# Optimization experiments

Hardware: AMD Instinct MI355X
Metric: run time of the kernel (lower is better)

## Reference

```python
import jax, jax.numpy as jnp
import numpy as np

D_MODEL = 1024
HID = 4096  # d_model * att_size
N_KEYS = 65536
TOP_K = 6


def setup_inputs() -> dict:
    root = jax.random.key(0)
    k0, k1, k2, k3, k4, k5 = jax.random.split(root, 6)
    s = 1.0 / np.sqrt(D_MODEL)
    return {
        "query": jax.random.normal(k0, (D_MODEL,), dtype=jnp.float32),
        "key_mat": jax.random.normal(k1, (N_KEYS, D_MODEL), dtype=jnp.float32),
        "Wq": jax.random.normal(k2, (HID, D_MODEL), dtype=jnp.float32) * s,
        "bq": jax.random.normal(k3, (HID,), dtype=jnp.float32) * s,
        "Wk": jax.random.normal(k4, (HID, D_MODEL), dtype=jnp.float32) * s,
        "bk": jax.random.normal(k5, (HID,), dtype=jnp.float32) * s,
    }


def reference(query, key_mat, Wq, bq, Wk, bk):
    # Linear projections (nn.Linear: x @ W^T + b)
    q = jnp.dot(Wq, query) + bq                 # [HID]
    k = jnp.dot(key_mat, Wk.T) + bk             # [N, HID]
    scores = jnp.dot(k, q)                      # [N]
    # The torch loop does k=6 sequential argmax + mask(-100000) + gather,
    # which (absent pathological -100000 scores) is exactly top-6 selection.
    _, idx = jax.lax.top_k(scores, TOP_K)       # [TOP_K]
    return jnp.mean(key_mat[idx], axis=0)       # [D_MODEL]
```

## Files before the change

### kernel.cpp

```cpp
#include <hip/hip_runtime.h>

#define DM    1024
#define HID   4096
#define NKEYS 65536
#define TOPK  6
#define NEGF  (-3.4e38f)

typedef float fvec4 __attribute__((ext_vector_type(4)));

__device__ __forceinline__ fvec4 nt_load4(const float* p) {
    return __builtin_nontemporal_load((const fvec4*)p);
}

__global__ __launch_bounds__(256) void qproj_kernel(const float* __restrict__ Wq,
                                                    const float* __restrict__ query,
                                                    const float* __restrict__ bq,
                                                    float* __restrict__ q) {
    const int wave = threadIdx.x >> 6;
    const int lane = threadIdx.x & 63;
    const int h = blockIdx.x * 4 + wave;
    const float* Wrow = Wq + (size_t)h * DM;
    const fvec4* __restrict__ qv = (const fvec4*)query;
    float acc = 0.f;
#pragma unroll
    for (int k = 0; k < 4; ++k) {
        fvec4 w = nt_load4(Wrow + (lane + k * 64) * 4);
        fvec4 x = qv[lane + k * 64];
        acc += w.x * x.x + w.y * x.y + w.z * x.z + w.w * x.w;
    }
#pragma unroll
    for (int off = 32; off > 0; off >>= 1) acc += __shfl_down(acc, off);
    if (lane == 0) q[h] = acc + bq[h];
}

__global__ __launch_bounds__(256) void vproj_kernel(const float* __restrict__ Wk,
                                                    const float* __restrict__ q,
                                                    float* __restrict__ v_part) {
    const int t  = threadIdx.x;
    const int b  = blockIdx.x;
    const int h0 = b * 16;
    fvec4 acc = {0.f, 0.f, 0.f, 0.f};
#pragma unroll 4
    for (int j = 0; j < 16; ++j) {
        const int h = h0 + j;
        const float qh = q[h];
        fvec4 w = nt_load4(Wk + (size_t)h * DM + t * 4);
        acc += w * qh;
    }
    *(fvec4*)(v_part + (size_t)b * DM + t * 4) = acc;
}

__global__ __launch_bounds__(64) void vreduce_kernel(const float* __restrict__ v_part,
                                                     float* __restrict__ v) {
    const int d = blockIdx.x * 64 + threadIdx.x;
    float acc = 0.f;
#pragma unroll 8
    for (int b = 0; b < 256; ++b) acc += v_part[(size_t)b * DM + d];
    v[d] = acc;
}

__global__ __launch_bounds__(256) void score_kernel(const float* __restrict__ key_mat,
                                                    const float* __restrict__ v,
                                                    float* __restrict__ scores) {
    const int wave = threadIdx.x >> 6;
    const int lane = threadIdx.x & 63;
    const int r = blockIdx.x * 4 + wave;
    const float* row = key_mat + (size_t)r * DM;
    const fvec4* __restrict__ vv = (const fvec4*)v;
    float acc = 0.f;
#pragma unroll
    for (int k = 0; k < 4; ++k) {
        fvec4 a = nt_load4(row + (lane + k * 64) * 4);
        fvec4 b = vv[lane + k * 64];
        acc += a.x * b.x + a.y * b.y + a.z * b.z + a.w * b.w;
    }
#pragma unroll
    for (int off = 32; off > 0; off >>= 1) acc += __shfl_down(acc, off);
    if (lane == 0) scores[r] = acc;
}

__global__ __launch_bounds__(256) void topk_stage1(const float* __restrict__ scores,
                                                   float* __restrict__ cand_v,
                                                   int* __restrict__ cand_i) {
    const int t = threadIdx.x, b = blockIdx.x;
    const int i = b * 256 + t;
    float cur = scores[i];

    __shared__ float wv[4];
    __shared__ int   wi[4];
    __shared__ float selv[TOPK];
    __shared__ int   seli[TOPK];

    for (int p = 0; p < TOPK; ++p) {
        float m = cur; int mi = i;
#pragma unroll
        for (int off = 32; off > 0; off >>= 1) {
            float ov = __shfl_down(m, off);
            int   oi = __shfl_down(mi, off);
            if (ov > m) { m = ov; mi = oi; }
        }
        const int lane = t & 63, w = t >> 6;
        if (lane == 0) { wv[w] = m; wi[w] = mi; }
        __syncthreads();
        if (t == 0) {
            float bm = wv[0]; int bix = wi[0];
#pragma unroll
            for (int j = 1; j < 4; ++j) if (wv[j] > bm) { bm = wv[j]; bix = wi[j]; }
            selv[p] = bm; seli[p] = bix;
        }
        __syncthreads();
        if (i == seli[p]) cur = NEGF;
    }
    if (t < TOPK) { cand_v[b * TOPK + t] = selv[t]; cand_i[b * TOPK + t] = seli[t]; }
}

__global__ __launch_bounds__(256) void topk_stage2_mean(const float* __restrict__ cand_v,
                                                        const int* __restrict__ cand_i,
                                                        const float* __restrict__ key_mat,
                                                        float* __restrict__ out) {
    const int t = threadIdx.x;
    const int NC = 256 * TOPK;

    __shared__ float sv[NC];
    __shared__ int   si[NC];
    __shared__ float wv[4];
    __shared__ int   wi[4];
    __shared__ int   sel[TOPK];

#pragma unroll
    for (int j = 0; j < TOPK; ++j) {
        sv[t + j * 256] = cand_v[t + j * 256];
        si[t + j * 256] = cand_i[t + j * 256];
    }
    __syncthreads();

    for (int p = 0; p < TOPK; ++p) {
        float m = NEGF; int mp = 0;
#pragma unroll
        for (int j = 0; j < TOPK; ++j) {
            const int pos = t * TOPK + j;
            const float val = sv[pos];
            if (val > m) { m = val; mp = pos; }
        }
#pragma unroll
        for (int off = 32; off > 0; off >>= 1) {
            float ov = __shfl_down(m, off);
            int   op = __shfl_down(mp, off);
            if (ov > m) { m = ov; mp = op; }
        }
        const int lane = t & 63, w = t >> 6;
        if (lane == 0) { wv[w] = m; wi[w] = mp; }
        __syncthreads();
        if (t == 0) {
            float bm = wv[0]; int bp = wi[0];
#pragma unroll
            for (int j = 1; j < 4; ++j) if (wv[j] > bm) { bm = wv[j]; bp = wi[j]; }
            sel[p] = si[bp];
            sv[bp] = NEGF;
        }
        __syncthreads();
    }

    fvec4 acc = {0.f, 0.f, 0.f, 0.f};
#pragma unroll
    for (int p = 0; p < TOPK; ++p) {
        fvec4 r = *(const fvec4*)(key_mat + (size_t)sel[p] * DM + t * 4);
        acc += r;
    }
    acc *= (1.0f / 6.0f);
    *(fvec4*)(out + t * 4) = acc;
}

extern "C" void kernel_launch(void* const* d_in, const int* in_sizes, int n_in,
                              void* d_out, int out_size, void* d_ws, size_t ws_size,
                              hipStream_t stream) {
    const float* query   = (const float*)d_in[0];
    const float* key_mat = (const float*)d_in[1];
    const float* Wq      = (const float*)d_in[2];
    const float* bq      = (const float*)d_in[3];
    const float* Wk      = (const float*)d_in[4];
    float* out = (float*)d_out;

    float* ws      = (float*)d_ws;
    float* q       = ws;
    float* v_part  = q + HID;
    float* v       = v_part + 256 * DM;
    float* scores  = v + DM;
    float* cand_v  = scores + NKEYS;
    int*   cand_i  = (int*)(cand_v + 256 * TOPK);

    qproj_kernel     <<<HID / 4,  256, 0, stream>>>(Wq, query, bq, q);
    vproj_kernel     <<<256,      256, 0, stream>>>(Wk, q, v_part);
    vreduce_kernel   <<<DM / 64,  64,  0, stream>>>(v_part, v);
    score_kernel     <<<NKEYS / 4,256, 0, stream>>>(key_mat, v, scores);
    topk_stage1      <<<256,      256, 0, stream>>>(scores, cand_v, cand_i);
    topk_stage2_mean <<<1,        256, 0, stream>>>(cand_v, cand_i, key_mat, out);
}
```

Baseline: 383.2 us.

## Fuse q/v projections and score with per-block top-k selection

Merges the query projection into the Wk-vector projection kernel, keeping the 16 q values each block needs in shared memory. Merges score computation with a first-stage top-6 per 64-row group, so the scores array is never written out. The final stage now does a register insertion sort over 1024*6 candidates before the shared-memory reduction. This removes two launches and a round trip of the scores through memory. In exchange each score block processes 64 rows and the final single-block stage scans more candidates.

New measurement: 402.9 us. +5.2%, slower.

```diff
diff --git a/kernel.cpp b/kernel.cpp
--- a/kernel.cpp
+++ b/kernel.cpp
@@ -12,42 +12,41 @@
     return __builtin_nontemporal_load((const fvec4*)p);
 }
 
-__global__ __launch_bounds__(256) void qproj_kernel(const float* __restrict__ Wq,
-                                                    const float* __restrict__ query,
-                                                    const float* __restrict__ bq,
-                                                    float* __restrict__ q) {
-    const int wave = threadIdx.x >> 6;
-    const int lane = threadIdx.x & 63;
-    const int h = blockIdx.x * 4 + wave;
-    const float* Wrow = Wq + (size_t)h * DM;
+__global__ __launch_bounds__(256) void proj_fused_kernel(const float* __restrict__ Wq,
+                                                         const float* __restrict__ query,
+                                                         const float* __restrict__ bq,
+                                                         const float* __restrict__ Wk,
+                                                         float* __restrict__ v_part) {
+    const int t = threadIdx.x, b = blockIdx.x;
+    const int wave = t >> 6, lane = t & 63;
+    const int h0 = b * 16;
+    __shared__ float qs[16];
+
     const fvec4* __restrict__ qv = (const fvec4*)query;
-    float acc = 0.f;
 #pragma unroll
-    for (int k = 0; k < 4; ++k) {
-        fvec4 w = nt_load4(Wrow + (lane + k * 64) * 4);
-        fvec4 x = qv[lane + k * 64];
-        acc += w.x * x.x + w.y * x.y + w.z * x.z + w.w * x.w;
+    for (int j = 0; j < 4; ++j) {
+        const int h = h0 + wave * 4 + j;
+        const float* Wrow = Wq + (size_t)h * DM;
+        float acc = 0.f;
+#pragma unroll
+        for (int k = 0; k < 4; ++k) {
+            fvec4 w = nt_load4(Wrow + (lane + k * 64) * 4);
+            fvec4 x = qv[lane + k * 64];
+            acc += w.x * x.x + w.y * x.y + w.z * x.z + w.w * x.w;
+        }
+#pragma unroll
+        for (int off = 32; off > 0; off >>= 1) acc += __shfl_down(acc, off);
+        if (lane == 0) qs[wave * 4 + j] = acc + bq[h];
     }
-#pragma unroll
-    for (int off = 32; off > 0; off >>= 1) acc += __shfl_down(acc, off);
-    if (lane == 0) q[h] = acc + bq[h];
-}
+    __syncthreads();
 
-__global__ __launch_bounds__(256) void vproj_kernel(const float* __restrict__ Wk,
-                                                    const float* __restrict__ q,
-                                                    float* __restrict__ v_part) {
-    const int t  = threadIdx.x;
-    const int b  = blockIdx.x;
-    const int h0 = b * 16;
-    fvec4 acc = {0.f, 0.f, 0.f, 0.f};
+    fvec4 acc4 = {0.f, 0.f, 0.f, 0.f};
 #pragma unroll 4
     for (int j = 0; j < 16; ++j) {
-        const int h = h0 + j;
-        const float qh = q[h];
-        fvec4 w = nt_load4(Wk + (size_t)h * DM + t * 4);
-        acc += w * qh;
+        fvec4 w = nt_load4(Wk + (size_t)(h0 + j) * DM + t * 4);
+        acc4 += w * qs[j];
     }
-    *(fvec4*)(v_part + (size_t)b * DM + t * 4) = acc;
+    *(fvec4*)(v_part + (size_t)b * DM + t * 4) = acc4;
 }
 
 __global__ __launch_bounds__(64) void vreduce_kernel(const float* __restrict__ v_part,
@@ -59,59 +58,51 @@
     v[d] = acc;
 }
 
-__global__ __launch_bounds__(256) void score_kernel(const float* __restrict__ key_mat,
-                                                    const float* __restrict__ v,
-                                                    float* __restrict__ scores) {
-    const int wave = threadIdx.x >> 6;
-    const int lane = threadIdx.x & 63;
-    const int r = blockIdx.x * 4 + wave;
-    const float* row = key_mat + (size_t)r * DM;
-    const fvec4* __restrict__ vv = (const fvec4*)v;
-    float acc = 0.f;
+__global__ __launch_bounds__(256) void score_topk_kernel(const float* __restrict__ key_mat,
+                                                         const float* __restrict__ v,
+                                                         float* __restrict__ cand_v,
+                                                         int* __restrict__ cand_i) {
+    const int t = threadIdx.x, g = blockIdx.x;
+    const int wave = t >> 6, lane = t & 63;
+    const int r0 = g * 64;
+
+    fvec4 vv[4];
 #pragma unroll
-    for (int k = 0; k < 4; ++k) {
-        fvec4 a = nt_load4(row + (lane + k * 64) * 4);
-        fvec4 b = vv[lane + k * 64];
-        acc += a.x * b.x + a.y * b.y + a.z * b.z + a.w * b.w;
+    for (int k = 0; k < 4; ++k) vv[k] = *(const fvec4*)(v + (lane + k * 64) * 4);
+
+    __shared__ float s_sc[64];
+#pragma unroll 2
+    for (int j = 0; j < 16; ++j) {
+        const int r = r0 + wave * 16 + j;
+        const float* row = key_mat + (size_t)r * DM;
+        float acc = 0.f;
+#pragma unroll
+        for (int k = 0; k < 4; ++k) {
+            fvec4 a = nt_load4(row + (lane + k * 64) * 4);
+            acc += a.x * vv[k].x + a.y * vv[k].y + a.z * vv[k].z + a.w * vv[k].w;
+        }
+#pragma unroll
+        for (int off = 32; off > 0; off >>= 1) acc += __shfl_down(acc, off);
+        if (lane == 0) s_sc[wave * 16 + j] = acc;
     }
+    __syncthreads();
+
+    if (t < 64) {
+        float val = s_sc[lane];
+        int idx = lane;
 #pragma unroll
-    for (int off = 32; off > 0; off >>= 1) acc += __shfl_down(acc, off);
-    if (lane == 0) scores[r] = acc;
-}
-
-__global__ __launch_bounds__(256) void topk_stage1(const float* __restrict__ scores,
-                                                   float* __restrict__ cand_v,
-                                                   int* __restrict__ cand_i) {
-    const int t = threadIdx.x, b = blockIdx.x;
-    const int i = b * 256 + t;
-    float cur = scores[i];
-
-    __shared__ float wv[4];
-    __shared__ int   wi[4];
-    __shared__ float selv[TOPK];
-    __shared__ int   seli[TOPK];
-
-    for (int p = 0; p < TOPK; ++p) {
-        float m = cur; int mi = i;
+        for (int p = 0; p < TOPK; ++p) {
+            float m = val; int mi = idx;
 #pragma unroll
-        for (int off = 32; off > 0; off >>= 1) {
-            float ov = __shfl_down(m, off);
-            int   oi = __shfl_down(mi, off);
-            if (ov > m) { m = ov; mi = oi; }
+            for (int off = 32; off > 0; off >>= 1) {
+                float ov = __shfl_xor(m, off);
+                int   oi = __shfl_xor(mi, off);
+                if (ov > m || (ov == m && oi < mi)) { m = ov; mi = oi; }
+            }
+            if (lane == p) { cand_v[g * TOPK + p] = m; cand_i[g * TOPK + p] = r0 + mi; }
+            if (lane == mi) val = NEGF;
         }
-        const int lane = t & 63, w = t >> 6;
-        if (lane == 0) { wv[w] = m; wi[w] = mi; }
-        __syncthreads();
-        if (t == 0) {
-            float bm = wv[0]; int bix = wi[0];
-#pragma unroll
-            for (int j = 1; j < 4; ++j) if (wv[j] > bm) { bm = wv[j]; bix = wi[j]; }
-            selv[p] = bm; seli[p] = bix;
-        }
-        __syncthreads();
-        if (i == seli[p]) cur = NEGF;
     }
-    if (t < TOPK) { cand_v[b * TOPK + t] = selv[t]; cand_i[b * TOPK + t] = seli[t]; }
 }
 
 __global__ __launch_bounds__(256) void topk_stage2_mean(const float* __restrict__ cand_v,
@@ -119,28 +110,37 @@
                                                         const float* __restrict__ key_mat,
                                                         float* __restrict__ out) {
     const int t = threadIdx.x;
-    const int NC = 256 * TOPK;
 
-    __shared__ float sv[NC];
-    __shared__ int   si[NC];
+    float bv[TOPK]; int bi[TOPK];
+#pragma unroll
+    for (int j = 0; j < TOPK; ++j) { bv[j] = NEGF; bi[j] = 0; }
+#pragma unroll 4
+    for (int j = 0; j < 24; ++j) {
+        const int pos = j * 256 + t;
+        const float s = cand_v[pos];
+        if (s > bv[TOPK - 1]) {
+            const int ii = cand_i[pos];
+            int p = TOPK - 1;
+            while (p > 0 && bv[p - 1] < s) { bv[p] = bv[p - 1]; bi[p] = bi[p - 1]; --p; }
+            bv[p] = s; bi[p] = ii;
+        }
+    }
+
+    __shared__ float sv[256 * TOPK];
+    __shared__ int   si[256 * TOPK];
     __shared__ float wv[4];
     __shared__ int   wi[4];
     __shared__ int   sel[TOPK];
-
 #pragma unroll
-    for (int j = 0; j < TOPK; ++j) {
-        sv[t + j * 256] = cand_v[t + j * 256];
-        si[t + j * 256] = cand_i[t + j * 256];
-    }
+    for (int j = 0; j < TOPK; ++j) { sv[t * TOPK + j] = bv[j]; si[t * TOPK + j] = bi[j]; }
     __syncthreads();
 
     for (int p = 0; p < TOPK; ++p) {
         float m = NEGF; int mp = 0;
 #pragma unroll
         for (int j = 0; j < TOPK; ++j) {
-            const int pos = t * TOPK + j;
-            const float val = sv[pos];
-            if (val > m) { m = val; mp = pos; }
+            const float val = sv[t * TOPK + j];
+            if (val > m) { m = val; mp = t * TOPK + j; }
         }
 #pragma unroll
         for (int off = 32; off > 0; off >>= 1) {
@@ -163,10 +163,8 @@
 
     fvec4 acc = {0.f, 0.f, 0.f, 0.f};
 #pragma unroll
-    for (int p = 0; p < TOPK; ++p) {
-        fvec4 r = *(const fvec4*)(key_mat + (size_t)sel[p] * DM + t * 4);
-        acc += r;
-    }
+    for (int p = 0; p < TOPK; ++p)
+        acc += *(const fvec4*)(key_mat + (size_t)sel[p] * DM + t * 4);
     acc *= (1.0f / 6.0f);
     *(fvec4*)(out + t * 4) = acc;
 }
@@ -182,17 +180,13 @@
     float* out = (float*)d_out;
 
     float* ws      = (float*)d_ws;
-    float* q       = ws;
-    float* v_part  = q + HID;
+    float* v_part  = ws;
     float* v       = v_part + 256 * DM;
-    float* scores  = v + DM;
-    float* cand_v  = scores + NKEYS;
-    int*   cand_i  = (int*)(cand_v + 256 * TOPK);
+    float* cand_v  = v + DM;
+    int*   cand_i  = (int*)(cand_v + 1024 * TOPK);
 
-    qproj_kernel     <<<HID / 4,  256, 0, stream>>>(Wq, query, bq, q);
-    vproj_kernel     <<<256,      256, 0, stream>>>(Wk, q, v_part);
+    proj_fused_kernel<<<256,      256, 0, stream>>>(Wq, query, bq, Wk, v_part);
     vreduce_kernel   <<<DM / 64,  64,  0, stream>>>(v_part, v);
-    score_kernel     <<<NKEYS / 4,256, 0, stream>>>(key_mat, v, scores);
-    topk_stage1      <<<256,      256, 0, stream>>>(scores, cand_v, cand_i);
+    score_topk_kernel<<<NKEYS/64, 256, 0, stream>>>(key_mat, v, cand_v, cand_i);
     topk_stage2_mean <<<1,        256, 0, stream>>>(cand_v, cand_i, key_mat, out);
 }
```
